# Kernel tuning notes

Measured on AMD Instinct MI355X. Metric: run time of the kernel, lower is better.

The kernel has to match this reference:

```python
import jax, jax.numpy as jnp
import numpy as np

GROUP = 4
ALPHA = 2.0


def sda(x, group=GROUP, alpha=ALPHA):
    # Per row: find FIRST group whose elements are all > 0 -> scale by alpha;
    # find FIRST group whose elements are all < 0 -> zero it. Masks are
    # computed on the original values, then applied.
    B, H = x.shape
    G = H // group
    xg = x.reshape(B, G, group)
    all_pos = jnp.all(xg > 0, axis=-1)            # [B, G]
    all_neg = jnp.all(xg < 0, axis=-1)            # [B, G]
    has_pos = jnp.any(all_pos, axis=-1, keepdims=True)   # [B, 1]
    has_neg = jnp.any(all_neg, axis=-1, keepdims=True)   # [B, 1]
    act_idx = jnp.argmax(all_pos, axis=-1, keepdims=True)    # first True
    inact_idx = jnp.argmax(all_neg, axis=-1, keepdims=True)  # first True
    gids = jnp.arange(G)[None, :]                 # [1, G]
    scale = jnp.ones((B, G), dtype=x.dtype)
    scale = jnp.where(has_pos & (gids == act_idx), jnp.asarray(alpha, x.dtype), scale)
    scale = jnp.where(has_neg & (gids == inact_idx), jnp.asarray(0.0, x.dtype), scale)
    return (xg * scale[:, :, None]).reshape(B, H)


def setup_inputs() -> dict:
    key = jax.random.key(0)
    ks = jax.random.split(key, 7)
    d_in, h1, h2, d_out = 1024, 4096, 4096, 1024
    x = jax.random.normal(ks[0], (8192, d_in), dtype=jnp.float32)
    def lin(kw, kb, fan_in, fan_out):
        bound = 1.0 / np.sqrt(fan_in)
        W = jax.random.uniform(kw, (fan_out, fan_in), jnp.float32, -bound, bound)
        b = jax.random.uniform(kb, (fan_out,), jnp.float32, -bound, bound)
        return W, b
    W1, b1 = lin(ks[1], ks[2], d_in, h1)
    W2, b2 = lin(ks[3], ks[4], h1, h2)
    W3, b3 = lin(ks[5], ks[6], h2, d_out)
    return {"x": x, "W1": W1, "b1": b1, "W2": W2, "b2": b2, "W3": W3, "b3": b3}


def reference(x, W1, b1, W2, b2, W3, b3):
    h = sda(x @ W1.T + b1)
    h = sda(h @ W2.T + b2)
    return h @ W3.T + b3
```

## Files before the change

### kernel.cpp

```cpp
#include <hip/hip_runtime.h>
#include <stdint.h>

using half8 = __attribute__((ext_vector_type(8))) _Float16;
using half4 = __attribute__((ext_vector_type(4))) _Float16;
using f32x4 = __attribute__((ext_vector_type(4))) float;

#define BM 256
#define BN 128
#define BK 32

__device__ __forceinline__ int swz(int row, int kb) {
  return (row << 6) + ((((kb >> 4) ^ ((row >> 1) & 3)) << 4) | (kb & 15));
}

#define GLD(src, dst)                                                          \
  __builtin_amdgcn_global_load_lds(                                            \
      (const __attribute__((address_space(1))) void*)(src),                    \
      (__attribute__((address_space(3))) void*)(dst), 16, 0, 0)

template <int MODE>
__global__ __launch_bounds__(1024, 4)
void gemm_tri(const _Float16* __restrict__ Ahi, const _Float16* __restrict__ Alo,
              const _Float16* __restrict__ Bhi, const _Float16* __restrict__ Blo,
              const float* __restrict__ bias,
              _Float16* __restrict__ Chi, _Float16* __restrict__ Clo,
              float* __restrict__ Cf, int M, int N, int K) {
  constexpr bool LO = (MODE < 2);
  constexpr int AHI = 0;
  constexpr int ALO = 16384;
  constexpr int BHI = LO ? 32768 : 16384;
  constexpr int BLO = 40960;
  constexpr int STG = LO ? 49152 : 24576;
  __shared__ char lds[3 * STG];

  const int tid = threadIdx.x;
  const int m0 = blockIdx.y * BM;
  const int n0 = blockIdx.x * BN;
  const int wave = tid >> 6, lane = tid & 63;
  const int wm = wave >> 1, wn = wave & 1;
  const int NK = K / BK;

  f32x4 acc_hi[2][4], acc_mid[2][4];
#pragma unroll
  for (int m = 0; m < 2; m++)
#pragma unroll
    for (int n = 0; n < 4; n++) { acc_hi[m][n] = (f32x4)0.0f; acc_mid[m][n] = (f32x4)0.0f; }

  const int srow = tid >> 2;
  const int kx = (tid & 3) ^ ((srow >> 1) & 3);
  const size_t aoff = (size_t)(m0 + srow) * K + kx * 8;
  const int brow = (tid & 511) >> 2;
  const size_t boff = (size_t)(n0 + brow) * K + kx * 8;

  auto STAGE = [&](int buf, int ks) {
    char* sb = lds + buf * STG;
    const size_t ko = (size_t)ks * BK;
    GLD(Ahi + aoff + ko, sb + AHI + (wave << 10));
    if constexpr (LO) {
      GLD(Alo + aoff + ko, sb + ALO + (wave << 10));
      if (wave < 8) GLD(Bhi + boff + ko, sb + BHI + (wave << 10));
      else          GLD(Blo + boff + ko, sb + BLO + ((wave - 8) << 10));
    } else {
      if (wave < 8) GLD(Bhi + boff + ko, sb + BHI + (wave << 10));
    }
  };

  auto COMPUTE = [&](int buf) {
    char* base = lds + buf * STG;
    const int kb = (lane >> 4) << 4;
    const int rl = lane & 15;
    half8 ah[2], al[2], bh[4], bl[4];
#pragma unroll
    for (int mi = 0; mi < 2; mi++) {
      int off = swz(wm * 32 + mi * 16 + rl, kb);
      ah[mi] = *(half8*)(base + AHI + off);
      if constexpr (LO) al[mi] = *(half8*)(base + ALO + off);
    }
#pragma unroll
    for (int ni = 0; ni < 4; ni++) {
      int off = swz(wn * 64 + ni * 16 + rl, kb);
      bh[ni] = *(half8*)(base + BHI + off);
      if constexpr (LO) bl[ni] = *(half8*)(base + BLO + off);
    }
    __builtin_amdgcn_s_setprio(1);
#pragma unroll
    for (int mi = 0; mi < 2; mi++)
#pragma unroll
      for (int ni = 0; ni < 4; ni++) {
        acc_hi[mi][ni] = __builtin_amdgcn_mfma_f32_16x16x32_f16(ah[mi], bh[ni], acc_hi[mi][ni], 0, 0, 0);
        if constexpr (LO) {
          acc_mid[mi][ni] = __builtin_amdgcn_mfma_f32_16x16x32_f16(ah[mi], bl[ni], acc_mid[mi][ni], 0, 0, 0);
          acc_mid[mi][ni] = __builtin_amdgcn_mfma_f32_16x16x32_f16(al[mi], bh[ni], acc_mid[mi][ni], 0, 0, 0);
        }
      }
    __builtin_amdgcn_s_setprio(0);
  };

  STAGE(0, 0);
  STAGE(1, 1);
  int cur = 0;
  for (int ks = 0; ks < NK; ++ks) {
    if (ks + 1 < NK) {
      if constexpr (LO) {
        asm volatile("s_waitcnt vmcnt(3)" ::: "memory");
      } else {
        if (wave < 8) asm volatile("s_waitcnt vmcnt(2)" ::: "memory");
        else          asm volatile("s_waitcnt vmcnt(1)" ::: "memory");
      }
    } else {
      asm volatile("s_waitcnt vmcnt(0)" ::: "memory");
    }
    __builtin_amdgcn_s_barrier();
    if (ks + 2 < NK) {
      int nbuf = cur + 2; if (nbuf >= 3) nbuf -= 3;
      STAGE(nbuf, ks + 2);
    }
    COMPUTE(cur);
    if (++cur == 3) cur = 0;
  }

  const int col_l = lane & 15, rgrp = lane >> 4;
#pragma unroll
  for (int ni = 0; ni < 4; ni++) {
    int col = n0 + wn * 64 + ni * 16 + col_l;
    float bv = bias[col];
#pragma unroll
    for (int mi = 0; mi < 2; mi++) {
      int rowb = m0 + wm * 32 + mi * 16 + rgrp * 4;
#pragma unroll
      for (int i = 0; i < 4; i++) {
        size_t idx = (size_t)(rowb + i) * N + col;
        if constexpr (MODE == 2) {
          Cf[idx] = acc_hi[mi][ni][i] + bv;
        } else {
          float c = acc_hi[mi][ni][i] + acc_mid[mi][ni][i] * (1.0f / 2048.0f) + bv;
          _Float16 hh = (_Float16)c;
          Chi[idx] = hh;
          if constexpr (MODE == 0) Clo[idx] = (_Float16)((c - (float)hh) * 2048.0f);
        }
      }
    }
  }
}

#define SQ_STG 32768

__global__ __launch_bounds__(1024, 4)
void gemm_sq(const _Float16* __restrict__ Ahi, const _Float16* __restrict__ Bhi,
             const float* __restrict__ bias, _Float16* __restrict__ Chi,
             int M, int N, int K) {
  __shared__ char lds[3 * SQ_STG];
  const int tid = threadIdx.x;
  const int m0 = blockIdx.y * 256;
  const int n0 = blockIdx.x * 256;
  const int wave = tid >> 6, lane = tid & 63;
  const int wm = wave >> 2, wn = wave & 3;
  const int NK = K / BK;

  f32x4 acc[4][4];
#pragma unroll
  for (int m = 0; m < 4; m++)
#pragma unroll
    for (int n = 0; n < 4; n++) acc[m][n] = (f32x4)0.0f;

  const int srow = tid >> 2;
  const int kx = (tid & 3) ^ ((srow >> 1) & 3);
  const size_t aoff = (size_t)(m0 + srow) * K + kx * 8;
  const size_t boff = (size_t)(n0 + srow) * K + kx * 8;

  const int kb = (lane >> 4) << 4;
  const int rl = lane & 15;
  int aswz[4], bswz[4];
#pragma unroll
  for (int i = 0; i < 4; i++) {
    aswz[i] = swz(wm * 64 + i * 16 + rl, kb);
    bswz[i] = 16384 + swz(wn * 64 + i * 16 + rl, kb);
  }

  auto STAGE = [&](int buf, int ks) {
    char* sb = lds + buf * SQ_STG + (wave << 10);
    const size_t ko = (size_t)ks * BK;
    GLD(Ahi + aoff + ko, sb);
    GLD(Bhi + boff + ko, sb + 16384);
  };

  auto COMPUTE = [&](int buf) {
    char* base = lds + buf * SQ_STG;
    half8 ah[4], bh[4];
#pragma unroll
    for (int i = 0; i < 4; i++) {
      ah[i] = *(half8*)(base + aswz[i]);
      bh[i] = *(half8*)(base + bswz[i]);
    }
    __builtin_amdgcn_s_setprio(1);
#pragma unroll
    for (int mi = 0; mi < 4; mi++)
#pragma unroll
      for (int ni = 0; ni < 4; ni++)
        acc[mi][ni] = __builtin_amdgcn_mfma_f32_16x16x32_f16(ah[mi], bh[ni], acc[mi][ni], 0, 0, 0);
    __builtin_amdgcn_s_setprio(0);
  };

  STAGE(0, 0);
  STAGE(1, 1);
  int cur = 0;
  for (int ks = 0; ks < NK; ++ks) {
    if (ks + 1 < NK) asm volatile("s_waitcnt vmcnt(2)" ::: "memory");
    else             asm volatile("s_waitcnt vmcnt(0)" ::: "memory");
    __builtin_amdgcn_s_barrier();
    if (ks + 2 < NK) {
      int nbuf = cur + 2; if (nbuf >= 3) nbuf -= 3;
      STAGE(nbuf, ks + 2);
    }
    COMPUTE(cur);
    if (++cur == 3) cur = 0;
  }

  const int col_l = lane & 15, rgrp = lane >> 4;
#pragma unroll
  for (int ni = 0; ni < 4; ni++) {
    int col = n0 + wn * 64 + ni * 16 + col_l;
    float bv = bias[col];
#pragma unroll
    for (int mi = 0; mi < 4; mi++) {
      int rowb = m0 + wm * 64 + mi * 16 + rgrp * 4;
#pragma unroll
      for (int i = 0; i < 4; i++)
        Chi[(size_t)(rowb + i) * N + col] = (_Float16)(acc[mi][ni][i] + bv);
    }
  }
}

__global__ __launch_bounds__(256)
void split_kernel(const float* __restrict__ X, _Float16* __restrict__ Xhi,
                  _Float16* __restrict__ Xlo, size_t n4) {
  size_t i = (size_t)blockIdx.x * 256 + threadIdx.x;
  const size_t stride = (size_t)gridDim.x * 256;
  for (; i < n4; i += stride) {
    float4 q = ((const float4*)X)[i];
    float a[4] = {q.x, q.y, q.z, q.w};
    half4 h, l;
#pragma unroll
    for (int j = 0; j < 4; ++j) {
      _Float16 hh = (_Float16)a[j];
      h[j] = hh;
      l[j] = (_Float16)((a[j] - (float)hh) * 2048.0f);
    }
    ((half4*)Xhi)[i] = h;
    if (Xlo) ((half4*)Xlo)[i] = l;
  }
}

__global__ __launch_bounds__(256)
void sda_fix(_Float16* __restrict__ Zhi, _Float16* __restrict__ Zlo,
             const float* __restrict__ Af,
             const _Float16* __restrict__ Ahi, const _Float16* __restrict__ Alo,
             const float* __restrict__ W, const float* __restrict__ bias,
             int H, int K, float TAU) {
  __shared__ int sPos[4], sNeg[4];
  __shared__ int nFix;
  __shared__ int fixIdx[96];
  __shared__ double sRed[4];
  __shared__ float sVal;
  const int row = blockIdx.x;
  _Float16* zh = Zhi + (size_t)row * H;
  _Float16* zl = Zlo ? Zlo + (size_t)row * H : nullptr;
  const int t = threadIdx.x;

  if (t == 0) nFix = 0;
  __syncthreads();

  float v[16];
  {
    half8 a0 = ((const half8*)zh)[t * 2], a1 = ((const half8*)zh)[t * 2 + 1];
    if (zl) {
      half8 b0 = ((const half8*)zl)[t * 2], b1 = ((const half8*)zl)[t * 2 + 1];
#pragma unroll
      for (int e = 0; e < 8; ++e) {
        v[e]     = (float)a0[e] + (float)b0[e] * (1.0f / 2048.0f);
        v[8 + e] = (float)a1[e] + (float)b1[e] * (1.0f / 2048.0f);
      }
    } else {
#pragma unroll
      for (int e = 0; e < 8; ++e) { v[e] = (float)a0[e]; v[8 + e] = (float)a1[e]; }
    }
  }

  bool cposa[4], pposa[4], cnega[4], pnega[4];
  int firstCpos = 0x7fffffff, firstCneg = 0x7fffffff;
#pragma unroll
  for (int j = 0; j < 4; ++j) {
    float g0 = v[j*4], g1 = v[j*4+1], g2 = v[j*4+2], g3 = v[j*4+3];
    cposa[j] = (g0 >  TAU) & (g1 >  TAU) & (g2 >  TAU) & (g3 >  TAU);
    pposa[j] = (g0 > -TAU) & (g1 > -TAU) & (g2 > -TAU) & (g3 > -TAU);
    cnega[j] = (g0 < -TAU) & (g1 < -TAU) & (g2 < -TAU) & (g3 < -TAU);
    pnega[j] = (g0 <  TAU) & (g1 <  TAU) & (g2 <  TAU) & (g3 <  TAU);
    int gi = (t << 2) + j;
    if (cposa[j] && gi < firstCpos) firstCpos = gi;
    if (cnega[j] && gi < firstCneg) firstCneg = gi;
  }
#pragma unroll
  for (int off = 32; off; off >>= 1) {
    firstCpos = min(firstCpos, __shfl_xor(firstCpos, off));
    firstCneg = min(firstCneg, __shfl_xor(firstCneg, off));
  }
  if ((t & 63) == 0) { sPos[t >> 6] = firstCpos; sNeg[t >> 6] = firstCneg; }
  __syncthreads();
  firstCpos = min(min(sPos[0], sPos[1]), min(sPos[2], sPos[3]));
  firstCneg = min(min(sNeg[0], sNeg[1]), min(sNeg[2], sNeg[3]));
  __syncthreads();

#pragma unroll
  for (int j = 0; j < 4; ++j) {
    int gi = (t << 2) + j;
    bool qual = (pposa[j] && !cposa[j] && gi <= firstCpos) ||
                (pnega[j] && !cnega[j] && gi <= firstCneg);
    if (qual) {
#pragma unroll
      for (int e = 0; e < 4; ++e) {
        if (fabsf(v[j*4+e]) < TAU) {
          int slot = atomicAdd(&nFix, 1);
          if (slot < 96) fixIdx[slot] = gi * 4 + e;
        }
      }
    }
  }
  __syncthreads();
  const int nf = min(nFix, 96);
  unsigned fixmask = 0;
  for (int i = 0; i < nf; ++i) {
    const int col = fixIdx[i];
    double s = 0.0;
    const float* wr = W + (size_t)col * K;
    if (Af) {
      const float* ar = Af + (size_t)row * K;
      for (int k = t; k < K; k += 256) s += (double)ar[k] * (double)wr[k];
    } else {
      const _Float16* ah = Ahi + (size_t)row * K;
      const _Float16* al = Alo + (size_t)row * K;
      for (int k = t; k < K; k += 256)
        s += ((double)(float)ah[k] + (double)(float)al[k] * (1.0 / 2048.0)) * (double)wr[k];
    }
#pragma unroll
    for (int off = 32; off; off >>= 1) s += __shfl_xor(s, off);
    if ((t & 63) == 0) sRed[t >> 6] = s;
    __syncthreads();
    if (t == 0)
      sVal = (float)(sRed[0] + sRed[1] + sRed[2] + sRed[3] + (double)bias[col]);
    __syncthreads();
    if ((col >> 4) == t) { v[col & 15] = sVal; fixmask |= 1u << (col & 15); }
    __syncthreads();
  }

  int fp = 0x7fffffff, fn = 0x7fffffff;
#pragma unroll
  for (int j = 0; j < 4; ++j) {
    bool ap = (v[j*4+0] > 0.f) & (v[j*4+1] > 0.f) & (v[j*4+2] > 0.f) & (v[j*4+3] > 0.f);
    bool an = (v[j*4+0] < 0.f) & (v[j*4+1] < 0.f) & (v[j*4+2] < 0.f) & (v[j*4+3] < 0.f);
    int g = (t << 2) + j;
    if (ap && g < fp) fp = g;
    if (an && g < fn) fn = g;
  }
#pragma unroll
  for (int off = 32; off; off >>= 1) {
    fp = min(fp, __shfl_xor(fp, off));
    fn = min(fn, __shfl_xor(fn, off));
  }
  if ((t & 63) == 0) { sPos[t >> 6] = fp; sNeg[t >> 6] = fn; }
  __syncthreads();
  fp = min(min(sPos[0], sPos[1]), min(sPos[2], sPos[3]));
  fn = min(min(sNeg[0], sNeg[1]), min(sNeg[2], sNeg[3]));
  const int act   = (fp == 0x7fffffff) ? -1 : fp;
  const int inact = (fn == 0x7fffffff) ? -1 : fn;

  unsigned chg = fixmask;
#pragma unroll
  for (int j = 0; j < 4; ++j) {
    int g = (t << 2) + j;
    if (g == act) {
      v[j*4+0] *= 2.f; v[j*4+1] *= 2.f; v[j*4+2] *= 2.f; v[j*4+3] *= 2.f;
      chg |= 0xFu << (j * 4);
    } else if (g == inact) {
      v[j*4+0] = v[j*4+1] = v[j*4+2] = v[j*4+3] = 0.f;
      chg |= 0xFu << (j * 4);
    }
  }
  while (chg) {
    int e = __ffs(chg) - 1; chg &= chg - 1;
    float val = v[e];
    _Float16 hh = (_Float16)val;
    zh[(t << 4) + e] = hh;
    if (zl) zl[(t << 4) + e] = (_Float16)((val - (float)hh) * 2048.0f);
  }
}

extern "C" void kernel_launch(void* const* d_in, const int* in_sizes, int n_in,
                              void* d_out, int out_size, void* d_ws, size_t ws_size,
                              hipStream_t stream) {
  const float* x  = (const float*)d_in[0];
  const float* W1 = (const float*)d_in[1];
  const float* b1 = (const float*)d_in[2];
  const float* W2 = (const float*)d_in[3];
  const float* b2 = (const float*)d_in[4];
  const float* W3 = (const float*)d_in[5];
  const float* b3 = (const float*)d_in[6];
  float* out = (float*)d_out;

  const int M = 8192, H = 4096, DIN = 1024, DOUT = 1024;

  char* w = (char*)d_ws;
  _Float16* Z1hi = (_Float16*)(w + 0);
  _Float16* Z1lo = (_Float16*)(w + ((size_t)64 << 20));
  _Float16* Z2hi = (_Float16*)(w + ((size_t)128 << 20));
  _Float16* W2hi = (_Float16*)(w + ((size_t)192 << 20));
  _Float16* xhi  = (_Float16*)(w + ((size_t)128 << 20));
  _Float16* xlo  = (_Float16*)(w + ((size_t)144 << 20));
  _Float16* W1hi = (_Float16*)(w + ((size_t)160 << 20));
  _Float16* W1lo = (_Float16*)(w + ((size_t)168 << 20));
  _Float16* W3hi = (_Float16*)(w + ((size_t)64 << 20));

  auto split = [&](const float* src, _Float16* hi, _Float16* lo, size_t n) {
    size_t n4 = n >> 2;
    int grid = (int)((n4 + 255) / 256);
    if (grid > 2048) grid = 2048;
    split_kernel<<<grid, 256, 0, stream>>>(src, hi, lo, n4);
  };
  split(x,  xhi,  xlo,  (size_t)M * DIN);
  split(W1, W1hi, W1lo, (size_t)H * DIN);
  split(W2, W2hi, (_Float16*)nullptr, (size_t)H * H);

  gemm_tri<0><<<dim3(H / BN, M / BM), dim3(1024), 0, stream>>>(
      xhi, xlo, W1hi, W1lo, b1, Z1hi, Z1lo, (float*)nullptr, M, H, DIN);
  sda_fix<<<M, 256, 0, stream>>>(Z1hi, Z1lo, x, (const _Float16*)nullptr,
                                 (const _Float16*)nullptr, W1, b1, H, DIN, 1e-4f);
  gemm_sq<<<dim3(H / 256, M / 256), dim3(1024), 0, stream>>>(
      Z1hi, W2hi, b2, Z2hi, M, H, H);
  sda_fix<<<M, 256, 0, stream>>>(Z2hi, (_Float16*)nullptr, (const float*)nullptr,
                                 Z1hi, Z1lo, W2, b2, H, H, 5e-3f);
  split(W3, W3hi, (_Float16*)nullptr, (size_t)DOUT * H);
  gemm_tri<2><<<dim3(DOUT / BN, M / BM), dim3(1024), 0, stream>>>(
      Z2hi, (const _Float16*)nullptr, W3hi, (const _Float16*)nullptr, b3,
      (_Float16*)nullptr, (_Float16*)nullptr, out, M, DOUT, H);
}
```

Measured before the change: 634.4 us.

## Add XCD-aware block remap, double-buffer square GEMM, fuse split kernels

Flattens GEMM grids and remaps block ids so consecutive tiles land on the same XCD, improving L2 reuse of shared A/B panels. Rewrites the square GEMM pipeline from a 3-stage BK=32 ring to a 2-buffer scheme with two half-stages per 64-wide K step, issuing loads between half computes. Fuses the four fp32-to-fp16 split launches into one kernel, moving the W3 split ahead of the GEMMs into a separate workspace region. The new pipeline waits for all loads each step, which may expose more memory latency.

```diff
diff --git a/kernel.cpp b/kernel.cpp
--- a/kernel.cpp
+++ b/kernel.cpp
@@ -11,6 +11,11 @@
 
 __device__ __forceinline__ int swz(int row, int kb) {
   return (row << 6) + ((((kb >> 4) ^ ((row >> 1) & 3)) << 4) | (kb & 15));
+}
+
+__device__ __forceinline__ int xcd_swz(int bid, int nwg) {
+  int cpx = nwg >> 3;
+  return (bid & 7) * cpx + (bid >> 3);
 }
 
 #define GLD(src, dst)                                                          \
@@ -24,7 +29,7 @@
               const _Float16* __restrict__ Bhi, const _Float16* __restrict__ Blo,
               const float* __restrict__ bias,
               _Float16* __restrict__ Chi, _Float16* __restrict__ Clo,
-              float* __restrict__ Cf, int M, int N, int K) {
+              float* __restrict__ Cf, int M, int N, int K, int nbx) {
   constexpr bool LO = (MODE < 2);
   constexpr int AHI = 0;
   constexpr int ALO = 16384;
@@ -34,8 +39,9 @@
   __shared__ char lds[3 * STG];
 
   const int tid = threadIdx.x;
-  const int m0 = blockIdx.y * BM;
-  const int n0 = blockIdx.x * BN;
+  const int sid = xcd_swz(blockIdx.x, gridDim.x);
+  const int m0 = (sid / nbx) * BM;
+  const int n0 = (sid % nbx) * BN;
   const int wave = tid >> 6, lane = tid & 63;
   const int wm = wave >> 1, wn = wave & 1;
   const int NK = K / BK;
@@ -143,19 +149,20 @@
   }
 }
 
-#define SQ_STG 32768
+#define SQ_BUF 65536
 
 __global__ __launch_bounds__(1024, 4)
 void gemm_sq(const _Float16* __restrict__ Ahi, const _Float16* __restrict__ Bhi,
              const float* __restrict__ bias, _Float16* __restrict__ Chi,
-             int M, int N, int K) {
-  __shared__ char lds[3 * SQ_STG];
+             int M, int N, int K, int nbx) {
+  __shared__ char lds[2 * SQ_BUF];
   const int tid = threadIdx.x;
-  const int m0 = blockIdx.y * 256;
-  const int n0 = blockIdx.x * 256;
+  const int sid = xcd_swz(blockIdx.x, gridDim.x);
+  const int m0 = (sid / nbx) * 256;
+  const int n0 = (sid % nbx) * 256;
   const int wave = tid >> 6, lane = tid & 63;
   const int wm = wave >> 2, wn = wave & 3;
-  const int NK = K / BK;
+  const int NE = K / 64;
 
   f32x4 acc[4][4];
 #pragma unroll
@@ -177,15 +184,15 @@
     bswz[i] = 16384 + swz(wn * 64 + i * 16 + rl, kb);
   }
 
-  auto STAGE = [&](int buf, int ks) {
-    char* sb = lds + buf * SQ_STG + (wave << 10);
+  auto STAGE_H = [&](int buf, int half, int ks) {
+    char* sb = lds + buf * SQ_BUF + half * 32768 + (wave << 10);
     const size_t ko = (size_t)ks * BK;
     GLD(Ahi + aoff + ko, sb);
     GLD(Bhi + boff + ko, sb + 16384);
   };
 
-  auto COMPUTE = [&](int buf) {
-    char* base = lds + buf * SQ_STG;
+  auto COMPUTE_H = [&](int buf, int half) {
+    char* base = lds + buf * SQ_BUF + half * 32768;
     half8 ah[4], bh[4];
 #pragma unroll
     for (int i = 0; i < 4; i++) {
@@ -201,19 +208,17 @@
     __builtin_amdgcn_s_setprio(0);
   };
 
-  STAGE(0, 0);
-  STAGE(1, 1);
-  int cur = 0;
-  for (int ks = 0; ks < NK; ++ks) {
-    if (ks + 1 < NK) asm volatile("s_waitcnt vmcnt(2)" ::: "memory");
-    else             asm volatile("s_waitcnt vmcnt(0)" ::: "memory");
+  STAGE_H(0, 0, 0);
+  STAGE_H(0, 1, 1);
+  int buf = 0;
+  for (int e = 0; e < NE; ++e) {
+    asm volatile("s_waitcnt vmcnt(0)" ::: "memory");
     __builtin_amdgcn_s_barrier();
-    if (ks + 2 < NK) {
-      int nbuf = cur + 2; if (nbuf >= 3) nbuf -= 3;
-      STAGE(nbuf, ks + 2);
-    }
-    COMPUTE(cur);
-    if (++cur == 3) cur = 0;
+    if (e + 1 < NE) STAGE_H(buf ^ 1, 0, 2 * e + 2);
+    COMPUTE_H(buf, 0);
+    if (e + 1 < NE) STAGE_H(buf ^ 1, 1, 2 * e + 3);
+    COMPUTE_H(buf, 1);
+    buf ^= 1;
   }
 
   const int col_l = lane & 15, rgrp = lane >> 4;
@@ -232,22 +237,34 @@
 }
 
 __global__ __launch_bounds__(256)
-void split_kernel(const float* __restrict__ X, _Float16* __restrict__ Xhi,
-                  _Float16* __restrict__ Xlo, size_t n4) {
+void split4_kernel(const float* __restrict__ s0, _Float16* __restrict__ h0,
+                   _Float16* __restrict__ l0, size_t n0,
+                   const float* __restrict__ s1, _Float16* __restrict__ h1,
+                   _Float16* __restrict__ l1, size_t n1,
+                   const float* __restrict__ s2, _Float16* __restrict__ h2,
+                   size_t n2,
+                   const float* __restrict__ s3, _Float16* __restrict__ h3,
+                   size_t n3) {
+  const size_t tot = n0 + n1 + n2 + n3;
   size_t i = (size_t)blockIdx.x * 256 + threadIdx.x;
   const size_t stride = (size_t)gridDim.x * 256;
-  for (; i < n4; i += stride) {
-    float4 q = ((const float4*)X)[i];
+  for (; i < tot; i += stride) {
+    const float* src; _Float16* hi; _Float16* lo; size_t j = i;
+    if (j < n0) { src = s0; hi = h0; lo = l0; }
+    else if ((j -= n0) < n1) { src = s1; hi = h1; lo = l1; }
+    else if ((j -= n1) < n2) { src = s2; hi = h2; lo = nullptr; }
+    else { j -= n2; src = s3; hi = h3; lo = nullptr; }
+    float4 q = ((const float4*)src)[j];
     float a[4] = {q.x, q.y, q.z, q.w};
     half4 h, l;
 #pragma unroll
-    for (int j = 0; j < 4; ++j) {
-      _Float16 hh = (_Float16)a[j];
-      h[j] = hh;
-      l[j] = (_Float16)((a[j] - (float)hh) * 2048.0f);
-    }
-    ((half4*)Xhi)[i] = h;
-    if (Xlo) ((half4*)Xlo)[i] = l;
+    for (int k = 0; k < 4; ++k) {
+      _Float16 hh = (_Float16)a[k];
+      h[k] = hh;
+      l[k] = (_Float16)((a[k] - (float)hh) * 2048.0f);
+    }
+    ((half4*)hi)[j] = h;
+    if (lo) ((half4*)lo)[j] = l;
   }
 }
 
@@ -417,28 +434,23 @@
   _Float16* xlo  = (_Float16*)(w + ((size_t)144 << 20));
   _Float16* W1hi = (_Float16*)(w + ((size_t)160 << 20));
   _Float16* W1lo = (_Float16*)(w + ((size_t)168 << 20));
-  _Float16* W3hi = (_Float16*)(w + ((size_t)64 << 20));
-
-  auto split = [&](const float* src, _Float16* hi, _Float16* lo, size_t n) {
-    size_t n4 = n >> 2;
-    int grid = (int)((n4 + 255) / 256);
-    if (grid > 2048) grid = 2048;
-    split_kernel<<<grid, 256, 0, stream>>>(src, hi, lo, n4);
-  };
-  split(x,  xhi,  xlo,  (size_t)M * DIN);
-  split(W1, W1hi, W1lo, (size_t)H * DIN);
-  split(W2, W2hi, (_Float16*)nullptr, (size_t)H * H);
-
-  gemm_tri<0><<<dim3(H / BN, M / BM), dim3(1024), 0, stream>>>(
-      xhi, xlo, W1hi, W1lo, b1, Z1hi, Z1lo, (float*)nullptr, M, H, DIN);
+  _Float16* W3hi = (_Float16*)(w + ((size_t)224 << 20));
+
+  split4_kernel<<<2048, 256, 0, stream>>>(
+      x,  xhi,  xlo,  (size_t)(M * DIN) >> 2,
+      W1, W1hi, W1lo, (size_t)(H * DIN) >> 2,
+      W2, W2hi,       (size_t)((size_t)H * H) >> 2,
+      W3, W3hi,       (size_t)(DOUT * H) >> 2);
+
+  gemm_tri<0><<<dim3((H / BN) * (M / BM)), dim3(1024), 0, stream>>>(
+      xhi, xlo, W1hi, W1lo, b1, Z1hi, Z1lo, (float*)nullptr, M, H, DIN, H / BN);
   sda_fix<<<M, 256, 0, stream>>>(Z1hi, Z1lo, x, (const _Float16*)nullptr,
                                  (const _Float16*)nullptr, W1, b1, H, DIN, 1e-4f);
-  gemm_sq<<<dim3(H / 256, M / 256), dim3(1024), 0, stream>>>(
-      Z1hi, W2hi, b2, Z2hi, M, H, H);
+  gemm_sq<<<dim3((H / 256) * (M / 256)), dim3(1024), 0, stream>>>(
+      Z1hi, W2hi, b2, Z2hi, M, H, H, H / 256);
   sda_fix<<<M, 256, 0, stream>>>(Z2hi, (_Float16*)nullptr, (const float*)nullptr,
                                  Z1hi, Z1lo, W2, b2, H, H, 5e-3f);
-  split(W3, W3hi, (_Float16*)nullptr, (size_t)DOUT * H);
-  gemm_tri<2><<<dim3(DOUT / BN, M / BM), dim3(1024), 0, stream>>>(
+  gemm_tri<2><<<dim3((DOUT / BN) * (M / BM)), dim3(1024), 0, stream>>>(
       Z2hi, (const _Float16*)nullptr, W3hi, (const _Float16*)nullptr, b3,
-      (_Float16*)nullptr, (_Float16*)nullptr, out, M, DOUT, H);
-}
+      (_Float16*)nullptr, (_Float16*)nullptr, out, M, DOUT, H, DOUT / BN);
+}
```

Result: faster. 613.6 us (median of 2 runs) (-3.3%).
